# Kernel tuning notes

Hardware: AMD Instinct MI355X
Metric: run time of the kernel (lower is better)

## Reference

```python
import jax, jax.numpy as jnp
import numpy as np

N, H = 8192, 1024

def setup_inputs() -> dict:
    key = jax.random.key(0)
    ks = jax.random.split(key, 7)
    s = 1.0 / np.sqrt(H)
    return {
        "x": jax.random.normal(ks[0], (N, H), dtype=jnp.float32),
        "Wq": jax.random.uniform(ks[1], (H, H), dtype=jnp.float32, minval=-s, maxval=s),
        "bq": jax.random.uniform(ks[2], (H,), dtype=jnp.float32, minval=-s, maxval=s),
        "Wk": jax.random.uniform(ks[3], (H, H), dtype=jnp.float32, minval=-s, maxval=s),
        "bk": jax.random.uniform(ks[4], (H,), dtype=jnp.float32, minval=-s, maxval=s),
        "Wv": jax.random.uniform(ks[5], (H, H), dtype=jnp.float32, minval=-s, maxval=s),
        "bv": jax.random.uniform(ks[6], (H,), dtype=jnp.float32, minval=-s, maxval=s),
    }

def reference(x, Wq, bq, Wk, bk, Wv, bv):
    # q/k/v projections: [N, H]
    q = x @ Wq + bq
    k = x @ Wk + bk
    v = x @ Wv + bv
    # full scores [N, N]; NOTE: original has no 1/sqrt(d) scaling
    scores = q @ k.T
    alpha = jax.nn.softmax(scores, axis=1)
    return alpha @ v
```

## Files before the change

kernel.cpp:

```cpp
#include <hip/hip_runtime.h>
#include <hip/hip_bf16.h>
#include <hip/hip_fp16.h>


typedef _Float16 f16x8 __attribute__((ext_vector_type(8)));
typedef float floatx4 __attribute__((ext_vector_type(4)));
typedef float floatx2 __attribute__((ext_vector_type(2)));
typedef unsigned short ushortx8 __attribute__((ext_vector_type(8)));

__device__ __forceinline__ unsigned short f2h(float f) {
  __half h = __float2half(f);
  return __builtin_bit_cast(unsigned short, h);
}
__device__ __forceinline__ float h2f(unsigned short u) {
  return __half2float(__builtin_bit_cast(__half, u));
}

__device__ __forceinline__ void async16(const void* g, void* l) {
  __builtin_amdgcn_global_load_lds(
      (__attribute__((address_space(1))) unsigned int*)(g),
      (__attribute__((address_space(3))) unsigned int*)(l),
      16, 0, 0);
}


__global__ __launch_bounds__(256) void conv_f32_f16(const float* __restrict__ in,
                                                    unsigned short* __restrict__ out,
                                                    long n) {
  long i = ((long)blockIdx.x * 256 + threadIdx.x) * 4;
  if (i + 3 < n) {
    float4 f = *(const float4*)(in + i);
    ushort4 o;
    o.x = f2h(f.x); o.y = f2h(f.y); o.z = f2h(f.z); o.w = f2h(f.w);
    *(ushort4*)(out + i) = o;
  }
}

__global__ __launch_bounds__(256) void transpose_f32_f16_3(const float* __restrict__ in0,
                                                           const float* __restrict__ in1,
                                                           const float* __restrict__ in2,
                                                           unsigned short* __restrict__ out,
                                                           int rows, int cols) {
  const float* in = (blockIdx.z == 0) ? in0 : (blockIdx.z == 1) ? in1 : in2;
  unsigned short* o = out + (size_t)blockIdx.z * rows * cols;
  __shared__ float tile[32][33];
  int bx = blockIdx.x * 32;
  int by = blockIdx.y * 32;
  int tx = threadIdx.x & 31, ty = threadIdx.x >> 5;
  #pragma unroll
  for (int yy = ty; yy < 32; yy += 8)
    tile[yy][tx] = in[(size_t)(by + yy) * cols + bx + tx];
  __syncthreads();
  #pragma unroll
  for (int yy = ty; yy < 32; yy += 8)
    o[(size_t)(bx + yy) * rows + by + tx] = f2h(tile[tx][yy]);
}

template <int MODE>
__global__ __launch_bounds__(256, 4)
void gemm_bt(const unsigned short* __restrict__ A,
             const unsigned short* __restrict__ B,
             int M, int Nn, int K,
             const float* __restrict__ b0, const float* __restrict__ b1,
             const float* __restrict__ b2,
             unsigned short* __restrict__ out) {
  if constexpr (MODE == 0) {
    B   += (size_t)blockIdx.z * Nn * K;
    out += (size_t)blockIdx.z * M * Nn;
  }
  const float* bias = (MODE != 0) ? nullptr
                      : (blockIdx.z == 0) ? b0 : (blockIdx.z == 1) ? b1 : b2;
  __shared__ unsigned short smem[128 * 136];
  unsigned short* As = smem;
  unsigned short* Bs = smem + 128 * 32;
  const int tid  = threadIdx.x;
  const int wave = tid >> 6;
  const int lane = tid & 63;
  const int wm = wave >> 1, wn = wave & 1;
  const int quad = lane >> 4, l16 = lane & 15;
  const long bm = (long)blockIdx.y * 128;
  const long bn = (long)blockIdx.x * 128;

  floatx4 acc[4][4] = {};

  const int srow = wave * 32 + (lane >> 2);
  const int scol = (lane & 3) * 8;
  const unsigned short* gA0 = A + (bm + srow) * (long)K + scol;
  const unsigned short* gA1 = gA0 + 16L * K;
  const unsigned short* gB0 = B + (bn + srow) * (long)K + scol;
  const unsigned short* gB1 = gB0 + 16L * K;
  unsigned short* lA0 = &As[(wave * 32) * 32];
  unsigned short* lA1 = &As[(wave * 32 + 16) * 32];
  unsigned short* lB0 = &Bs[(wave * 32) * 32];
  unsigned short* lB1 = &Bs[(wave * 32 + 16) * 32];

  for (int kk = 0; kk < K; kk += 32) {
    async16(gA0 + kk, lA0);
    async16(gA1 + kk, lA1);
    async16(gB0 + kk, lB0);
    async16(gB1 + kk, lB1);
    __syncthreads();
    f16x8 af[4], bfv[4];
    #pragma unroll
    for (int i = 0; i < 4; ++i) {
      af[i]  = *reinterpret_cast<const f16x8*>(&As[(wm * 64 + i * 16 + l16) * 32 + quad * 8]);
      bfv[i] = *reinterpret_cast<const f16x8*>(&Bs[(wn * 64 + i * 16 + l16) * 32 + quad * 8]);
    }
    #pragma unroll
    for (int i = 0; i < 4; ++i)
      #pragma unroll
      for (int j = 0; j < 4; ++j)
        acc[i][j] = __builtin_amdgcn_mfma_f32_16x16x32_f16(af[i], bfv[j], acc[i][j], 0, 0, 0);
    __syncthreads();
  }
  #pragma unroll
  for (int i = 0; i < 4; ++i) {
    const int row0 = wm * 64 + i * 16 + quad * 4;
    #pragma unroll
    for (int j = 0; j < 4; ++j) {
      const int col = wn * 64 + j * 16 + l16;
      const float cb = (MODE == 0) ? bias[bn + col] : 0.0f;
      #pragma unroll
      for (int r = 0; r < 4; ++r)
        smem[(row0 + r) * 136 + col] = f2h(acc[i][j][r] + cb);
    }
  }
  __syncthreads();
  #pragma unroll
  for (int u = 0; u < 8; ++u) {
    const int chunk = u * 256 + tid;
    const int row = chunk >> 4;
    const int cc = chunk & 15;
    const ushortx8 val = *reinterpret_cast<const ushortx8*>(&smem[row * 136 + cc * 8]);
    *reinterpret_cast<ushortx8*>(&out[(bm + row) * (long)Nn + bn + cc * 8]) = val;
  }
}

__global__ __launch_bounds__(256) void softmax_compact(unsigned short* __restrict__ S,
                                                       int* __restrict__ nnz, int n) {
  const int wid  = threadIdx.x >> 6;
  const int lane = threadIdx.x & 63;
  const int row  = blockIdx.x * 4 + wid;
  unsigned short* prow = S + ((size_t)row << 13);

  ushortx8 c[16];
  #pragma unroll
  for (int u = 0; u < 16; ++u)
    c[u] = *reinterpret_cast<const ushortx8*>(&prow[u * 512 + lane * 8]);

  float m0 = -1e30f, m1 = -1e30f, m2 = -1e30f, m3 = -1e30f;
  #pragma unroll
  for (int u = 0; u < 16; ++u) {
    m0 = fmaxf(m0, fmaxf(h2f(c[u][0]), h2f(c[u][4])));
    m1 = fmaxf(m1, fmaxf(h2f(c[u][1]), h2f(c[u][5])));
    m2 = fmaxf(m2, fmaxf(h2f(c[u][2]), h2f(c[u][6])));
    m3 = fmaxf(m3, fmaxf(h2f(c[u][3]), h2f(c[u][7])));
  }
  float m = fmaxf(fmaxf(m0, m1), fmaxf(m2, m3));
  #pragma unroll
  for (int off = 32; off > 0; off >>= 1)
    m = fmaxf(m, __shfl_xor(m, off, 64));

  float s0 = 0.f, s1 = 0.f, s2 = 0.f, s3 = 0.f;
  #pragma unroll
  for (int u = 0; u < 16; ++u) {
    s0 += __expf(h2f(c[u][0]) - m) + __expf(h2f(c[u][4]) - m);
    s1 += __expf(h2f(c[u][1]) - m) + __expf(h2f(c[u][5]) - m);
    s2 += __expf(h2f(c[u][2]) - m) + __expf(h2f(c[u][6]) - m);
    s3 += __expf(h2f(c[u][3]) - m) + __expf(h2f(c[u][7]) - m);
  }
  float s = (s0 + s1) + (s2 + s3);
  #pragma unroll
  for (int off = 32; off > 0; off >>= 1)
    s += __shfl_xor(s, off, 64);
  const float inv = 1.0f / s;

  unsigned int* pairs = (unsigned int*)prow;
  const int cap = 4096 - 8;
  int base = 0;
  #pragma unroll
  for (int u = 0; u < 16; ++u) {
    #pragma unroll
    for (int e = 0; e < 8; ++e) {
      const unsigned short hh = f2h(__expf(h2f(c[u][e]) - m) * inv);
      const unsigned long long mask = __ballot(hh != 0);
      if (hh) {
        const int pos = base + (int)__popcll(mask & ((1ull << lane) - 1ull));
        if (pos < cap)
          pairs[pos] = ((unsigned)(u * 512 + lane * 8 + e) << 16) | hh;
      }
      base += (int)__popcll(mask);
    }
  }
  const int c_cl = base < cap ? base : cap;
  const int padded = (c_cl + 7) & ~7;
  if (lane < padded - c_cl) pairs[c_cl + lane] = 0u;
  if (lane == 0) nnz[row] = padded;
}

__global__ __launch_bounds__(256) void pv_sliced(const unsigned short* __restrict__ S,
                                                 const int* __restrict__ nnz,
                                                 const unsigned short* __restrict__ v,
                                                 float* __restrict__ out,
                                                 int n) {
  const int wave = threadIdx.x >> 6;
  const int lane = threadIdx.x & 63;
  const int colbase = blockIdx.x * 128 + lane * 2;
  const unsigned colbyte = (unsigned)colbase * 2;
  const char* __restrict__ vb = (const char*)v;
  const char* __restrict__ sb = (const char*)S;

  #pragma unroll 1
  for (int r = 0; r < 4; ++r) {
    const int row = blockIdx.y + ((wave << 2) + r) * 512;
    int craw = nnz[row];
    craw = craw < 0 ? 0 : (craw > 4096 ? 4096 : craw);
    const int cnt = __builtin_amdgcn_readfirstlane(craw);
    const unsigned rowbase = (unsigned)row << 14;
    const unsigned pend = rowbase + 16384 - 32;
    unsigned poff = rowbase;
    uint4 q0 = *(const uint4*)(sb + poff);
    uint4 q1 = *(const uint4*)(sb + poff + 16);
    float a0 = 0.f, a1 = 0.f;
    for (int j = 0; j < cnt; j += 8) {
      const unsigned pn = (poff + 32 <= pend) ? poff + 32 : pend;
      const uint4 n0 = *(const uint4*)(sb + pn);
      const uint4 n1 = *(const uint4*)(sb + pn + 16);
      const unsigned p[8] = {q0.x, q0.y, q0.z, q0.w, q1.x, q1.y, q1.z, q1.w};
      #pragma unroll
      for (int u = 0; u < 8; ++u) {
        const ushort2 vv = *(const ushort2*)(vb + (((p[u] & 0xffff0000u) >> 5) + colbyte));
        const float w = h2f((unsigned short)(p[u] & 0xffffu));
        a0 += w * h2f(vv.x);
        a1 += w * h2f(vv.y);
      }
      q0 = n0; q1 = n1; poff = pn;
    }
    floatx2 o = {a0, a1};
    __builtin_nontemporal_store(o, (floatx2*)(out + ((size_t)row << 10) + colbase));
  }
}

extern "C" void kernel_launch(void* const* d_in, const int* in_sizes, int n_in,
                              void* d_out, int out_size, void* d_ws, size_t ws_size,
                              hipStream_t stream) {
  const int N = 8192, H = 1024;
  const float* x  = (const float*)d_in[0];
  const float* Wq = (const float*)d_in[1];
  const float* bq = (const float*)d_in[2];
  const float* Wk = (const float*)d_in[3];
  const float* bk = (const float*)d_in[4];
  const float* Wv = (const float*)d_in[5];
  const float* bv = (const float*)d_in[6];

  char* p = (char*)d_ws;
  unsigned short* xh  = (unsigned short*)p; p += (size_t)N * H * 2;
  unsigned short* WT  = (unsigned short*)p; p += (size_t)3 * H * H * 2;
  unsigned short* qkv = (unsigned short*)p; p += (size_t)3 * N * H * 2;
  unsigned short* S   = (unsigned short*)p; p += (size_t)N * N * 2;
  int*            nnz = (int*)p;            p += (size_t)N * 4;
  if ((size_t)(p - (char*)d_ws) > ws_size) return;
  unsigned short* qh = qkv;
  unsigned short* kh = qkv + (size_t)N * H;
  unsigned short* vh = qkv + (size_t)2 * N * H;

  conv_f32_f16<<<(N * H / 4 + 255) / 256, 256, 0, stream>>>(x, xh, (long)N * H);
  transpose_f32_f16_3<<<dim3(H / 32, H / 32, 3), 256, 0, stream>>>(Wq, Wk, Wv, WT, H, H);

  gemm_bt<0><<<dim3(H / 128, N / 128, 3), 256, 0, stream>>>(xh, WT, N, H, H,
                                                            bq, bk, bv, qkv);

  gemm_bt<1><<<dim3(N / 128, N / 128), 256, 0, stream>>>(qh, kh, N, N, H,
                                                         nullptr, nullptr, nullptr, S);
  softmax_compact<<<N / 4, 256, 0, stream>>>(S, nnz, N);
  pv_sliced<<<dim3(8, N / 16), 256, 0, stream>>>(S, nnz, vh, (float*)d_out, N);
}
```

Baseline: 542.9 us.

## Add dedicated 256x256-tile pipelined GEMM for the QK^T score matrix

Replaces the generic 128x128 gemm_bt used for the N x N score product with a specialised 512-thread kernel that computes 256x256 tiles. It uses a 4-stage async global-to-LDS pipeline with explicit vmcnt waits, XOR-swizzled LDS layout to avoid bank conflicts, a grouped block-index swizzle for L2 locality, and raised wave priority around the MFMA bursts. The aim is more data reuse per LDS load and better latency hiding for the dominant GEMM, at the cost of heavy register pressure (32 accumulators per thread) and hardcoded problem dimensions.

```diff
diff --git a/kernel.cpp b/kernel.cpp
--- a/kernel.cpp
+++ b/kernel.cpp
@@ -56,7 +56,6 @@
     o[(size_t)(bx + yy) * rows + by + tx] = f2h(tile[tx][yy]);
 }
 
-template <int MODE>
 __global__ __launch_bounds__(256, 4)
 void gemm_bt(const unsigned short* __restrict__ A,
              const unsigned short* __restrict__ B,
@@ -64,12 +63,9 @@
              const float* __restrict__ b0, const float* __restrict__ b1,
              const float* __restrict__ b2,
              unsigned short* __restrict__ out) {
-  if constexpr (MODE == 0) {
-    B   += (size_t)blockIdx.z * Nn * K;
-    out += (size_t)blockIdx.z * M * Nn;
-  }
-  const float* bias = (MODE != 0) ? nullptr
-                      : (blockIdx.z == 0) ? b0 : (blockIdx.z == 1) ? b1 : b2;
+  B   += (size_t)blockIdx.z * Nn * K;
+  out += (size_t)blockIdx.z * M * Nn;
+  const float* bias = (blockIdx.z == 0) ? b0 : (blockIdx.z == 1) ? b1 : b2;
   __shared__ unsigned short smem[128 * 136];
   unsigned short* As = smem;
   unsigned short* Bs = smem + 128 * 32;
@@ -119,7 +115,7 @@
     #pragma unroll
     for (int j = 0; j < 4; ++j) {
       const int col = wn * 64 + j * 16 + l16;
-      const float cb = (MODE == 0) ? bias[bn + col] : 0.0f;
+      const float cb = bias[bn + col];
       #pragma unroll
       for (int r = 0; r < 4; ++r)
         smem[(row0 + r) * 136 + col] = f2h(acc[i][j][r] + cb);
@@ -133,6 +129,113 @@
     const int cc = chunk & 15;
     const ushortx8 val = *reinterpret_cast<const ushortx8*>(&smem[row * 136 + cc * 8]);
     *reinterpret_cast<ushortx8*>(&out[(bm + row) * (long)Nn + bn + cc * 8]) = val;
+  }
+}
+
+__global__ __launch_bounds__(512, 2)
+void gemm256(const unsigned short* __restrict__ A,
+             const unsigned short* __restrict__ B,
+             unsigned short* __restrict__ out) {
+  constexpr int Nd = 8192;
+  constexpr int K = 1024;
+  __shared__ unsigned short smem[65536];
+  const int tid  = threadIdx.x;
+  const int lane = tid & 63;
+  const int wave = tid >> 6;
+  const int wm = wave >> 2, wn = wave & 3;
+  const int quad = lane >> 4, l16 = lane & 15;
+
+  const unsigned lin = blockIdx.y * gridDim.x + blockIdx.x;
+  const unsigned nb  = gridDim.x * gridDim.y;
+  const unsigned swz = (lin & 7u) * (nb >> 3) + (lin >> 3);
+  const long bm = (long)(swz >> 5) * 256;
+  const long bn = (long)(swz & 31u) * 256;
+
+  floatx4 acc[8][4] = {};
+
+  const int c0 = tid, c1 = tid + 512;
+  const int r0 = c0 >> 2, r1 = c1 >> 2;
+  const int sl0 = (c0 & 3) ^ ((r0 >> 1) & 3);
+  const int sl1 = (c1 & 3) ^ ((r1 >> 1) & 3);
+  const unsigned short* gA0 = A + (bm + r0) * (long)K + sl0 * 8;
+  const unsigned short* gA1 = A + (bm + r1) * (long)K + sl1 * 8;
+  const unsigned short* gB0 = B + (bn + r0) * (long)K + sl0 * 8;
+  const unsigned short* gB1 = B + (bn + r1) * (long)K + sl1 * 8;
+  const int ldsw0 = (c0 & ~63) * 8;
+  const int ldsw1 = (c1 & ~63) * 8;
+
+  auto STAGE = [&](int kt) {
+    unsigned short* bufA = smem + (kt & 3) * 16384;
+    unsigned short* bufB = bufA + 8192;
+    const int ko = kt * 32;
+    async16(gA0 + ko, bufA + ldsw0);
+    async16(gA1 + ko, bufA + ldsw1);
+    async16(gB0 + ko, bufB + ldsw0);
+    async16(gB1 + ko, bufB + ldsw1);
+  };
+
+  STAGE(0); STAGE(1); STAGE(2);
+
+  for (int kt = 0; kt < 32; ++kt) {
+    const unsigned short* bufA = smem + (kt & 3) * 16384;
+    const unsigned short* bufB = bufA + 8192;
+    if (kt <= 29)      asm volatile("s_waitcnt vmcnt(8)" ::: "memory");
+    else if (kt == 30) asm volatile("s_waitcnt vmcnt(4)" ::: "memory");
+    else               asm volatile("s_waitcnt vmcnt(0)" ::: "memory");
+    __builtin_amdgcn_s_barrier();
+    __builtin_amdgcn_sched_barrier(0);
+    if (kt + 3 < 32) STAGE(kt + 3);
+
+    f16x8 bf[4];
+    #pragma unroll
+    for (int j = 0; j < 4; ++j) {
+      const int R = wn * 64 + j * 16 + l16;
+      bf[j] = *reinterpret_cast<const f16x8*>(
+          bufB + R * 32 + ((quad ^ ((R >> 1) & 3)) * 8));
+    }
+    #pragma unroll
+    for (int qd = 0; qd < 4; ++qd) {
+      const int R0 = wm * 128 + (2 * qd) * 16 + l16;
+      const int R1 = R0 + 16;
+      const f16x8 a0 = *reinterpret_cast<const f16x8*>(
+          bufA + R0 * 32 + ((quad ^ ((R0 >> 1) & 3)) * 8));
+      const f16x8 a1 = *reinterpret_cast<const f16x8*>(
+          bufA + R1 * 32 + ((quad ^ ((R1 >> 1) & 3)) * 8));
+      __builtin_amdgcn_s_setprio(1);
+      #pragma unroll
+      for (int j = 0; j < 4; ++j) {
+        acc[2 * qd][j] =
+            __builtin_amdgcn_mfma_f32_16x16x32_f16(a0, bf[j], acc[2 * qd][j], 0, 0, 0);
+        acc[2 * qd + 1][j] =
+            __builtin_amdgcn_mfma_f32_16x16x32_f16(a1, bf[j], acc[2 * qd + 1][j], 0, 0, 0);
+      }
+      __builtin_amdgcn_s_setprio(0);
+    }
+  }
+
+  __syncthreads();
+  #pragma unroll
+  for (int half = 0; half < 2; ++half) {
+    if (wm == half) {
+      #pragma unroll
+      for (int i = 0; i < 8; ++i)
+        #pragma unroll
+        for (int j = 0; j < 4; ++j)
+          #pragma unroll
+          for (int r = 0; r < 4; ++r)
+            smem[(i * 16 + quad * 4 + r) * 258 + wn * 64 + j * 16 + l16] =
+                f2h(acc[i][j][r]);
+    }
+    __syncthreads();
+    #pragma unroll
+    for (int s = 0; s < 8; ++s) {
+      const int chunk = s * 512 + tid;
+      const int row = chunk >> 5, cc = chunk & 31;
+      *reinterpret_cast<ushortx8*>(
+          out + (bm + half * 128 + row) * (long)Nd + bn + cc * 8) =
+          *reinterpret_cast<const ushortx8*>(smem + row * 258 + cc * 8);
+    }
+    __syncthreads();
   }
 }
 
@@ -267,11 +370,11 @@
   conv_f32_f16<<<(N * H / 4 + 255) / 256, 256, 0, stream>>>(x, xh, (long)N * H);
   transpose_f32_f16_3<<<dim3(H / 32, H / 32, 3), 256, 0, stream>>>(Wq, Wk, Wv, WT, H, H);
 
-  gemm_bt<0><<<dim3(H / 128, N / 128, 3), 256, 0, stream>>>(xh, WT, N, H, H,
-                                                            bq, bk, bv, qkv);
-
-  gemm_bt<1><<<dim3(N / 128, N / 128), 256, 0, stream>>>(qh, kh, N, N, H,
-                                                         nullptr, nullptr, nullptr, S);
+  gemm_bt<<<dim3(H / 128, N / 128, 3), 256, 0, stream>>>(xh, WT, N, H, H,
+                                                         bq, bk, bv, qkv);
+
+  gemm256<<<dim3(N / 256, N / 256), 512, 0, stream>>>(qh, kh, S);
+
   softmax_compact<<<N / 4, 256, 0, stream>>>(S, nnz, N);
   pv_sliced<<<dim3(8, N / 16), 256, 0, stream>>>(S, nnz, vh, (float*)d_out, N);
 }
```

Result: no change. 552.6 us (+1.8%).
